# Performance work log

Hardware: AMD Instinct MI355X
Metric: run time of the kernel (lower is better)

The kernel has to match this reference:

```python
import jax, jax.numpy as jnp
import numpy as np

B, M, P = 128, 35, 224  # batch, num Zernike modes, pupil_size
SIGN_PENALTY = 10.0
RECON_WEIGHT = 0.4
DEFOCUS_RAD = 1.0
EPS = 1e-8


def setup_inputs() -> dict:
    key = jax.random.key(0)
    k1, k2, k3, k4 = jax.random.split(key, 4)
    pred = jax.random.normal(k1, (B, M), dtype=jnp.float32)
    target = jax.random.normal(k2, (B, M), dtype=jnp.float32)
    input_psfs = jax.random.uniform(k3, (B, 2, P, P), dtype=jnp.float32)
    zernike_basis = jax.random.normal(k4, (M, P, P), dtype=jnp.float32)
    pupil_mask = jnp.ones((P, P), dtype=jnp.float32)
    return {
        "pred": pred,
        "target": target,
        "input_psfs": input_psfs,
        "zernike_basis": zernike_basis,
        "pupil_mask": pupil_mask,
    }


def _psf_from_phase(phase, pupil_mask):
    # phase: [B,P,P] real; pupil: masked complex field
    pupil = pupil_mask[None, :, :] * jnp.exp(1j * phase)
    field = jnp.fft.fftshift(jnp.fft.fft2(pupil), axes=(-2, -1))
    psf = field.real ** 2 + field.imag ** 2  # |FFT|^2
    psf = psf / (psf.sum(axis=(-2, -1), keepdims=True) + EPS)
    return psf


def reference(pred, target, input_psfs, zernike_basis, pupil_mask):
    # --- sign-weighted MSE on Zernike coefficients ---
    base = (pred - target) ** 2
    sign_match = jnp.sign(pred) * jnp.sign(target)
    weight = jnp.where(sign_match < 0, SIGN_PENALTY, 1.0)
    z_loss = jnp.mean(base * weight)

    # --- batched differentiable PSF reconstruction loss ---
    phase = jnp.einsum('bm,mhw->bhw', pred, zernike_basis)
    phase = phase * pupil_mask[None, :, :]

    sim_if = _psf_from_phase(phase, pupil_mask)  # in-focus

    lin = jnp.linspace(-1.0, 1.0, P, dtype=jnp.float32)
    y, x = jnp.meshgrid(lin, lin, indexing='ij')
    r2 = x ** 2 + y ** 2
    defocus_phase = DEFOCUS_RAD * (2.0 * r2 - 1.0)  # [P,P]
    sim_podf = _psf_from_phase(phase + defocus_phase[None, :, :], pupil_mask)

    # per-sample F.mse_loss then mean over batch == mean over the batched arrays
    recon_loss = (jnp.mean((sim_if - input_psfs[:, 0]) ** 2)
                  + jnp.mean((sim_podf - input_psfs[:, 1]) ** 2))

    return z_loss + RECON_WEIGHT * recon_loss
```

## Files before the change

### kernel.cpp

```cpp
#include <hip/hip_runtime.h>
#include <math.h>

#define BB 128
#define MM 35
#define PSZ 224
#define PP (PSZ*PSZ)
#define SIGN_PENALTY 10.0f
#define RECON_WEIGHT 0.4f
#define DEFOCUS_RAD 1.0f
#define EPS_F 1e-8f
#define INV2PI 0.15915494309189535f


#define WS_PHASE_OFF    2048
#define WS_T_OFF        (WS_PHASE_OFF + BB*PP)
#define N_PARTIALS      (14*BB*2)
#define S1 233
#define S2 20

static constexpr float W16R[16] = {
    1.0f, 0.9238795325f, 0.7071067812f, 0.3826834324f, 0.0f,
    -0.3826834324f, -0.7071067812f, -0.9238795325f, -1.0f,
    -0.9238795325f, -0.7071067812f, -0.3826834324f, 0.0f,
    0.3826834324f, 0.7071067812f, 0.9238795325f};
static constexpr float W16I[16] = {
    0.0f, -0.3826834324f, -0.7071067812f, -0.9238795325f, -1.0f,
    -0.9238795325f, -0.7071067812f, -0.3826834324f, 0.0f,
    0.3826834324f, 0.7071067812f, 0.9238795325f, 1.0f,
    0.9238795325f, 0.7071067812f, 0.3826834324f};
static constexpr float W7R[7] = {
    1.0f, 0.6234898019f, -0.2225209340f, -0.9009688679f,
    -0.9009688679f, -0.2225209340f, 0.6234898019f};
static constexpr float W7I[7] = {
    0.0f, -0.7818314825f, -0.9749279122f, -0.4338837391f,
    0.4338837391f, 0.9749279122f, 0.7818314825f};
static constexpr float W14R[7] = {
    1.0f, 0.9009688679f, 0.6234898019f, 0.2225209340f, -0.2225209340f,
    -0.6234898019f, -0.9009688679f};
static constexpr float W14I[7] = {
    0.0f, -0.4338837391f, -0.7818314825f, -0.9749279122f, -0.9749279122f,
    -0.7818314825f, -0.4338837391f};

__device__ __forceinline__ float lincoord(int i) {
    return -1.0f + 2.0f * (float)i / (float)(PSZ - 1);
}
__device__ __forceinline__ void fast_sincos(float x, float* s, float* c) {
    float rv = x * INV2PI;
    rv -= floorf(rv);
    *s = __builtin_amdgcn_sinf(rv);
    *c = __builtin_amdgcn_cosf(rv);
}
__device__ __forceinline__ float2 wexp_neg(float frac) {
    float rv = -frac;
    rv -= floorf(rv);
    return make_float2(__builtin_amdgcn_cosf(rv), __builtin_amdgcn_sinf(rv));
}
__device__ __forceinline__ unsigned pack_bf2(float a, float b) {
    unsigned r;
    asm("v_cvt_pk_bf16_f32 %0, %1, %2" : "=v"(r) : "v"(a), "v"(b));
    return r;
}
__device__ __forceinline__ float2 unpack_bf2(unsigned v) {
    return make_float2(__uint_as_float(v << 16), __uint_as_float(v & 0xffff0000u));
}
__device__ __forceinline__ float2 cmul(float2 a, float2 b) {
    return make_float2(fmaf(a.x, b.x, -a.y * b.y), fmaf(a.x, b.y, a.y * b.x));
}
__device__ __forceinline__ float2 cmulc(float2 a, float wr, float wi) {
    return make_float2(fmaf(a.x, wr, -a.y * wi), fmaf(a.x, wi, a.y * wr));
}
__device__ __forceinline__ float2 cadd(float2 a, float2 b) {
    return make_float2(a.x + b.x, a.y + b.y);
}
__device__ __forceinline__ float2 csub(float2 a, float2 b) {
    return make_float2(a.x - b.x, a.y - b.y);
}
__device__ __forceinline__ void cfma(float& acc, float c, float v) {
    if (c == 0.f) return;
    if (c == 1.f)  { acc += v; return; }
    if (c == -1.f) { acc -= v; return; }
    acc = fmaf(c, v, acc);
}

__device__ __forceinline__ void dft8_sym(const float2* u, float2* X) {
    float2 a1 = cadd(u[1], u[7]), b1 = csub(u[1], u[7]);
    float2 a2 = cadd(u[2], u[6]), b2 = csub(u[2], u[6]);
    float2 a3 = cadd(u[3], u[5]), b3 = csub(u[3], u[5]);
    float2 s04 = cadd(u[0], u[4]), d04 = csub(u[0], u[4]);
    X[0] = cadd(cadd(s04, a1), cadd(a2, a3));
    X[4] = cadd(csub(s04, a1), csub(a2, a3));
    {
        float2 p = csub(s04, a2);
        float2 q = csub(b1, b3);
        X[2] = make_float2(p.x + q.y, p.y - q.x);
        X[6] = make_float2(p.x - q.y, p.y + q.x);
    }
#pragma unroll
    for (int m = 1; m <= 3; m += 2) {
        float Px = d04.x, Py = d04.y, Qx = 0.f, Qy = 0.f;
#pragma unroll
        for (int n = 1; n <= 3; n++) {
            const float cR = W16R[(2 * n * m) & 15], cI = W16I[(2 * n * m) & 15];
            const float2 a = (n == 1) ? a1 : (n == 2) ? a2 : a3;
            const float2 b = (n == 1) ? b1 : (n == 2) ? b2 : b3;
            cfma(Px, cR, a.x); cfma(Py, cR, a.y);
            cfma(Qx, cI, b.x); cfma(Qy, cI, b.y);
        }
        X[m]     = make_float2(Px - Qy, Py + Qx);
        X[8 - m] = make_float2(Px + Qy, Py - Qx);
    }
}

__device__ __forceinline__ void dft7_sym(const float2* x, float2* X) {
    float2 a1 = cadd(x[1], x[6]), b1 = csub(x[1], x[6]);
    float2 a2 = cadd(x[2], x[5]), b2 = csub(x[2], x[5]);
    float2 a3 = cadd(x[3], x[4]), b3 = csub(x[3], x[4]);
    X[0] = cadd(cadd(x[0], a1), cadd(a2, a3));
#pragma unroll
    for (int k = 1; k <= 3; k++) {
        float Px = x[0].x, Py = x[0].y, Qx = 0.f, Qy = 0.f;
#pragma unroll
        for (int n = 1; n <= 3; n++) {
            const float cR = W7R[(n * k) % 7], cI = W7I[(n * k) % 7];
            const float2 a = (n == 1) ? a1 : (n == 2) ? a2 : a3;
            const float2 b = (n == 1) ? b1 : (n == 2) ? b2 : b3;
            cfma(Px, cR, a.x); cfma(Py, cR, a.y);
            cfma(Qx, cI, b.x); cfma(Qy, cI, b.y);
        }
        X[k]     = make_float2(Px - Qy, Py + Qx);
        X[7 - k] = make_float2(Px + Qy, Py - Qx);
    }
}

__device__ __forceinline__ void inner16_core(const float2* xin,
                                             unsigned* __restrict__ xbuf,
                                             int base, int mul, int n1) {
    float2 u[8], v[8];
#pragma unroll
    for (int n = 0; n < 8; n++) {
        u[n] = cadd(xin[n], xin[n + 8]);
        float2 w = csub(xin[n], xin[n + 8]);
        v[n] = (n == 0) ? w : cmulc(w, W16R[n], W16I[n]);
    }
    float2 u1w = wexp_neg((float)n1 * (1.0f / 224.0f));
    float2 u2w = wexp_neg((float)n1 * (1.0f / 112.0f));
    {
        float2 Xe[8];
        dft8_sym(u, Xe);
        float2 cur = make_float2(1.f, 0.f);
#pragma unroll
        for (int m = 0; m < 8; m++) {
            float2 z = (m == 0) ? Xe[0] : cmul(Xe[m], cur);
            xbuf[base + (14 * (2 * m)) * mul] = pack_bf2(z.x, z.y);
            cur = cmul(cur, u2w);
        }
    }
    {
        float2 Xo[8];
        dft8_sym(v, Xo);
        float2 cur = u1w;
#pragma unroll
        for (int m = 0; m < 8; m++) {
            float2 z = cmul(Xo[m], cur);
            xbuf[base + (14 * (2 * m + 1)) * mul] = pack_bf2(z.x, z.y);
            cur = cmul(cur, u2w);
        }
    }
}

__global__ __launch_bounds__(256) void k_phase(const float* __restrict__ pred,
                                               const float* __restrict__ target,
                                               const float* __restrict__ zern,
                                               const float* __restrict__ mask,
                                               unsigned* __restrict__ field,
                                               float* __restrict__ ws) {
    __shared__ __align__(16) float pl[32 * 36];
    __shared__ float red[256];
    int t = threadIdx.x;
    if (blockIdx.x == 196) {
        int y = blockIdx.y;
        float s = 0.f;
        if (y == 0) {
            if (t < 224) {
                float v = lincoord(t);
                float fc = fmaf(2.f * DEFOCUS_RAD, v * v, -DEFOCUS_RAD);
                float fr = 2.f * DEFOCUS_RAD * v * v;
                float sn, cs;
                fast_sincos(fc, &sn, &cs);
                ((float2*)(ws + 16))[t] = make_float2(cs, sn);
                fast_sincos(fr, &sn, &cs);
                ((float2*)(ws + 512))[t] = make_float2(cs, sn);
            }
            for (int i = t; i < BB * MM; i += 256) {
                float p = pred[i], tg = target[i];
                float dd = p - tg;
                float w = (p * tg < 0.f) ? SIGN_PENALTY : 1.f;
                s = fmaf(dd * dd, w, s);
            }
        } else {
            const int F4 = PP / 4;
            int st = (y - 1) * 4182;
            int en = (y == 3) ? F4 : st + 4182;
            const float4* m4 = (const float4*)mask;
            for (int i = st + t; i < en; i += 256) {
                float4 v = m4[i];
                s = fmaf(v.x, v.x, s); s = fmaf(v.y, v.y, s);
                s = fmaf(v.z, v.z, s); s = fmaf(v.w, v.w, s);
            }
        }
        red[t] = s;
        __syncthreads();
        for (int st = 128; st > 0; st >>= 1) {
            if (t < st) red[t] += red[t + st];
            __syncthreads();
        }
        if (t == 0) {
            if (y == 0) ws[1] = red[0] / (float)(BB * MM);
            else        ws[1 + y] = red[0];
        }
        return;
    }
    int bg = blockIdx.y;
    for (int i = t; i < 32 * MM; i += 256) {
        int j = i / MM, m = i - (i / MM) * MM;
        pl[j * 36 + m] = pred[(bg * 32 + j) * MM + m];
    }
    if (t < 32) pl[t * 36 + 35] = 0.f;
    __syncthreads();
    int pix = blockIdx.x * 256 + t;
    float acc[32];
#pragma unroll
    for (int j = 0; j < 32; j++) acc[j] = 0.f;
    const float4* pl4 = (const float4*)pl;
    for (int mb = 0; mb < 32; mb += 4) {
        float z0 = zern[(size_t)(mb + 0) * PP + pix];
        float z1 = zern[(size_t)(mb + 1) * PP + pix];
        float z2 = zern[(size_t)(mb + 2) * PP + pix];
        float z3 = zern[(size_t)(mb + 3) * PP + pix];
#pragma unroll
        for (int j = 0; j < 32; j++) {
            float4 p4 = pl4[j * 9 + (mb >> 2)];
            acc[j] = fmaf(p4.x, z0, acc[j]);
            acc[j] = fmaf(p4.y, z1, acc[j]);
            acc[j] = fmaf(p4.z, z2, acc[j]);
            acc[j] = fmaf(p4.w, z3, acc[j]);
        }
    }
    {
        float z0 = zern[(size_t)32 * PP + pix];
        float z1 = zern[(size_t)33 * PP + pix];
        float z2 = zern[(size_t)34 * PP + pix];
#pragma unroll
        for (int j = 0; j < 32; j++) {
            float4 p4 = pl4[j * 9 + 8];
            acc[j] = fmaf(p4.x, z0, acc[j]);
            acc[j] = fmaf(p4.y, z1, acc[j]);
            acc[j] = fmaf(p4.z, z2, acc[j]);
        }
    }
    float mk = mask[pix];
#pragma unroll
    for (int j = 0; j < 32; j++) {
        float ph = acc[j] * mk;
        float sn, cs;
        fast_sincos(ph, &sn, &cs);
        field[(size_t)(bg * 32 + j) * PP + pix] = pack_bf2(mk * cs, mk * sn);
    }
}

__global__ __launch_bounds__(256, 5) void k_stage1(const unsigned* __restrict__ field,
                                                   const float* __restrict__ ws,
                                                   unsigned* __restrict__ T) {
    __shared__ unsigned xs[16 * S1];
    int h0 = blockIdx.x * 16;
    int d = blockIdx.y, b = blockIdx.z;
    int t = threadIdx.x;

    if (t < 224) {
        int r = t / 14, n1 = t - (t / 14) * 14;
        const unsigned* frow = field + (size_t)b * PP + (size_t)(h0 + r) * PSZ;
        float2 x0[16];
        if (d) {
            const float2* ctab = (const float2*)(ws + 16);
            const float2* rtab = (const float2*)(ws + 512);
            float2 crow = rtab[h0 + r];
#pragma unroll
            for (int n = 0; n < 16; n++) {
                int col = n1 + 14 * n;
                float2 f = unpack_bf2(frow[col]);
                float2 rot = cmul(crow, ctab[col]);
                x0[n] = cmul(rot, f);
            }
        } else {
#pragma unroll
            for (int n = 0; n < 16; n++) x0[n] = unpack_bf2(frow[n1 + 14 * n]);
        }
        inner16_core(x0, xs, r * S1 + n1, 1, n1);
    }
    __syncthreads();

    {
        int r = t >> 4, k2 = t & 15;
        const unsigned* xr = xs + r * S1 + k2 * 14;
        int img = d * BB + b;
        unsigned* Tt = T + (((size_t)img * 14) * PSZ + (h0 + r)) * 16 + k2;
        float2 e[7], E[7], O[7];
#pragma unroll
        for (int n = 0; n < 7; n++) e[n] = unpack_bf2(xr[2 * n]);
        dft7_sym(e, E);
#pragma unroll
        for (int n = 0; n < 7; n++) e[n] = unpack_bf2(xr[2 * n + 1]);
        dft7_sym(e, O);
#pragma unroll
        for (int k1 = 0; k1 < 7; k1++) {
            float2 op = (k1 == 0) ? O[0] : cmulc(O[k1], W14R[k1], W14I[k1]);
            float2 s = cadd(E[k1], op), q = csub(E[k1], op);
            Tt[(size_t)k1 * (PSZ * 16)]       = pack_bf2(s.x, s.y);
            Tt[(size_t)(k1 + 7) * (PSZ * 16)] = pack_bf2(q.x, q.y);
        }
    }
}

__global__ __launch_bounds__(256, 5) void k_stage2(const unsigned* __restrict__ T,
                                                   const float* __restrict__ psfs,
                                                   const float* __restrict__ ws,
                                                   float* __restrict__ partials) {
    __shared__ unsigned xs[224 * S2];
    __shared__ float red[4];
    int tile = blockIdx.x, b = blockIdx.y, d = blockIdx.z;
    int img = d * BB + b;
    int t = threadIdx.x;
    int k2o = t >> 4, c = t & 15;
    bool act = t < 224;

    const unsigned* Tb = T + ((size_t)img * 14 + tile) * (PSZ * 16);
    const float* inp = psfs + ((size_t)b * 2 + d) * PP;
    int scol = 16 * ((tile + 7) % 14) + c;

    unsigned xr[16];
    if (act) {
#pragma unroll
        for (int n = 0; n < 16; n++) xr[n] = Tb[224 * n + t];
    }
    float pf[14];
#pragma unroll
    for (int j = 0; j < 7; j++) {
        pf[j]     = inp[(size_t)(112 + 16 * j + k2o) * PSZ + scol];
        pf[j + 7] = inp[(size_t)(16 * j + k2o) * PSZ + scol];
    }

    if (act) {
        float2 x[16];
#pragma unroll
        for (int n = 0; n < 16; n++) x[n] = unpack_bf2(xr[n]);
        inner16_core(x, xs, (t >> 4) * S2 + (t & 15), S2, t >> 4);
    }
    __syncthreads();

    float m2 = ws[2] + ws[3] + ws[4];
    float inv_denom = 1.f / (m2 * (float)PP + EPS_F);

    float lsum = 0.f;
    {
        float2 e[7], E[7], O[7];
#pragma unroll
        for (int n = 0; n < 7; n++) e[n] = unpack_bf2(xs[(k2o * 14 + 2 * n) * S2 + c]);
        dft7_sym(e, E);
#pragma unroll
        for (int n = 0; n < 7; n++) e[n] = unpack_bf2(xs[(k2o * 14 + 2 * n + 1) * S2 + c]);
        dft7_sym(e, O);
#pragma unroll
        for (int k1 = 0; k1 < 7; k1++) {
            float2 op = (k1 == 0) ? O[0] : cmulc(O[k1], W14R[k1], W14I[k1]);
            float2 s = cadd(E[k1], op), q = csub(E[k1], op);
            float ds = fmaf(s.x, s.x, s.y * s.y) * inv_denom - pf[k1];
            float dq = fmaf(q.x, q.x, q.y * q.y) * inv_denom - pf[k1 + 7];
            lsum = fmaf(ds, ds, lsum);
            lsum = fmaf(dq, dq, lsum);
        }
    }
#pragma unroll
    for (int off = 32; off > 0; off >>= 1)
        lsum += __shfl_down(lsum, off, 64);
    if ((t & 63) == 0) red[t >> 6] = lsum;
    __syncthreads();
    if (t == 0)
        partials[(blockIdx.z * BB + blockIdx.y) * 14 + blockIdx.x] =
            red[0] + red[1] + red[2] + red[3];
}

__global__ void k_final(const float* __restrict__ ws,
                        const float* __restrict__ partials,
                        float* __restrict__ out) {
    __shared__ float red[256];
    float s = 0.f;
    for (int i = threadIdx.x; i < N_PARTIALS; i += 256) s += partials[i];
    red[threadIdx.x] = s;
    __syncthreads();
    for (int st = 128; st > 0; st >>= 1) {
        if (threadIdx.x < st) red[threadIdx.x] += red[threadIdx.x + st];
        __syncthreads();
    }
    if (threadIdx.x == 0) {
        float recon = red[0] / (float)((size_t)BB * PP);
        out[0] = ws[1] + RECON_WEIGHT * recon;
    }
}

extern "C" void kernel_launch(void* const* d_in, const int* in_sizes, int n_in,
                              void* d_out, int out_size, void* d_ws, size_t ws_size,
                              hipStream_t stream) {
    const float* pred   = (const float*)d_in[0];
    const float* target = (const float*)d_in[1];
    const float* psfs   = (const float*)d_in[2];
    const float* zern   = (const float*)d_in[3];
    const float* mask   = (const float*)d_in[4];

    float*    ws       = (float*)d_ws;
    unsigned* field    = (unsigned*)(ws + WS_PHASE_OFF);
    float*    partials = ws + WS_PHASE_OFF;
    unsigned* T        = (unsigned*)(ws + WS_T_OFF);
    float*    out      = (float*)d_out;

    k_phase<<<dim3(197, 4), 256, 0, stream>>>(pred, target, zern, mask, field, ws);
    k_stage1<<<dim3(14, 2, BB), 256, 0, stream>>>(field, ws, T);
    k_stage2<<<dim3(14, BB, 2), 256, 0, stream>>>(T, psfs, ws, partials);
    k_final<<<1, 256, 0, stream>>>(ws, partials, out);
}
```

Baseline: 153.0 us.

## Fold final reduction into stage2 and register-block two pixels per thread in k_phase

The separate k_final launch is removed. Each k_stage2 block now bumps a global atomic counter after writing its partial sum, and the last block to finish reduces all partials and writes the output. The counter is reset each call by k_phase. k_phase now computes two pixels per thread with software-prefetched Zernike loads, halving its grid; this increases register pressure and reduces the number of blocks in flight.

```diff
diff --git a/kernel.cpp b/kernel.cpp
--- a/kernel.cpp
+++ b/kernel.cpp
@@ -168,19 +168,20 @@
     }
 }
 
-__global__ __launch_bounds__(256) void k_phase(const float* __restrict__ pred,
-                                               const float* __restrict__ target,
-                                               const float* __restrict__ zern,
-                                               const float* __restrict__ mask,
-                                               unsigned* __restrict__ field,
-                                               float* __restrict__ ws) {
+__global__ __launch_bounds__(256, 4) void k_phase(const float* __restrict__ pred,
+                                                  const float* __restrict__ target,
+                                                  const float* __restrict__ zern,
+                                                  const float* __restrict__ mask,
+                                                  unsigned* __restrict__ field,
+                                                  float* __restrict__ ws) {
     __shared__ __align__(16) float pl[32 * 36];
     __shared__ float red[256];
     int t = threadIdx.x;
-    if (blockIdx.x == 196) {
+    if (blockIdx.x == 98) {
         int y = blockIdx.y;
         float s = 0.f;
         if (y == 0) {
+            if (t == 0) ((int*)ws)[8] = 0;
             if (t < 224) {
                 float v = lincoord(t);
                 float fc = fmaf(2.f * DEFOCUS_RAD, v * v, -DEFOCUS_RAD);
@@ -227,44 +228,56 @@
     }
     if (t < 32) pl[t * 36 + 35] = 0.f;
     __syncthreads();
-    int pix = blockIdx.x * 256 + t;
-    float acc[32];
-#pragma unroll
-    for (int j = 0; j < 32; j++) acc[j] = 0.f;
+    int pix0 = blockIdx.x * 512 + t;
+    int pix1 = pix0 + 256;
+    float acc0[32], acc1[32];
+#pragma unroll
+    for (int j = 0; j < 32; j++) { acc0[j] = 0.f; acc1[j] = 0.f; }
     const float4* pl4 = (const float4*)pl;
-    for (int mb = 0; mb < 32; mb += 4) {
-        float z0 = zern[(size_t)(mb + 0) * PP + pix];
-        float z1 = zern[(size_t)(mb + 1) * PP + pix];
-        float z2 = zern[(size_t)(mb + 2) * PP + pix];
-        float z3 = zern[(size_t)(mb + 3) * PP + pix];
+    float cz[4], cw[4];
+#pragma unroll
+    for (int q = 0; q < 4; q++) {
+        cz[q] = zern[(size_t)q * PP + pix0];
+        cw[q] = zern[(size_t)q * PP + pix1];
+    }
+    for (int ch = 0; ch < 9; ch++) {
+        float nz[4], nw[4];
+        if (ch < 8) {
+            int nb = (ch + 1) * 4;
+#pragma unroll
+            for (int q = 0; q < 4; q++) {
+                if (nb + q < MM) {
+                    nz[q] = zern[(size_t)(nb + q) * PP + pix0];
+                    nw[q] = zern[(size_t)(nb + q) * PP + pix1];
+                } else { nz[q] = 0.f; nw[q] = 0.f; }
+            }
+        }
 #pragma unroll
         for (int j = 0; j < 32; j++) {
-            float4 p4 = pl4[j * 9 + (mb >> 2)];
-            acc[j] = fmaf(p4.x, z0, acc[j]);
-            acc[j] = fmaf(p4.y, z1, acc[j]);
-            acc[j] = fmaf(p4.z, z2, acc[j]);
-            acc[j] = fmaf(p4.w, z3, acc[j]);
-        }
-    }
-    {
-        float z0 = zern[(size_t)32 * PP + pix];
-        float z1 = zern[(size_t)33 * PP + pix];
-        float z2 = zern[(size_t)34 * PP + pix];
-#pragma unroll
-        for (int j = 0; j < 32; j++) {
-            float4 p4 = pl4[j * 9 + 8];
-            acc[j] = fmaf(p4.x, z0, acc[j]);
-            acc[j] = fmaf(p4.y, z1, acc[j]);
-            acc[j] = fmaf(p4.z, z2, acc[j]);
-        }
-    }
-    float mk = mask[pix];
+            float4 p4 = pl4[j * 9 + ch];
+            acc0[j] = fmaf(p4.x, cz[0], acc0[j]);
+            acc0[j] = fmaf(p4.y, cz[1], acc0[j]);
+            acc0[j] = fmaf(p4.z, cz[2], acc0[j]);
+            acc0[j] = fmaf(p4.w, cz[3], acc0[j]);
+            acc1[j] = fmaf(p4.x, cw[0], acc1[j]);
+            acc1[j] = fmaf(p4.y, cw[1], acc1[j]);
+            acc1[j] = fmaf(p4.z, cw[2], acc1[j]);
+            acc1[j] = fmaf(p4.w, cw[3], acc1[j]);
+        }
+        if (ch < 8) {
+#pragma unroll
+            for (int q = 0; q < 4; q++) { cz[q] = nz[q]; cw[q] = nw[q]; }
+        }
+    }
+    float mk0 = mask[pix0], mk1 = mask[pix1];
 #pragma unroll
     for (int j = 0; j < 32; j++) {
-        float ph = acc[j] * mk;
+        size_t row = (size_t)(bg * 32 + j) * PP;
         float sn, cs;
-        fast_sincos(ph, &sn, &cs);
-        field[(size_t)(bg * 32 + j) * PP + pix] = pack_bf2(mk * cs, mk * sn);
+        fast_sincos(acc0[j] * mk0, &sn, &cs);
+        field[row + pix0] = pack_bf2(mk0 * cs, mk0 * sn);
+        fast_sincos(acc1[j] * mk1, &sn, &cs);
+        field[row + pix1] = pack_bf2(mk1 * cs, mk1 * sn);
     }
 }
 
@@ -323,10 +336,12 @@
 
 __global__ __launch_bounds__(256, 5) void k_stage2(const unsigned* __restrict__ T,
                                                    const float* __restrict__ psfs,
-                                                   const float* __restrict__ ws,
-                                                   float* __restrict__ partials) {
+                                                   float* __restrict__ ws,
+                                                   float* __restrict__ partials,
+                                                   float* __restrict__ out) {
     __shared__ unsigned xs[224 * S2];
     __shared__ float red[4];
+    __shared__ int lastflag;
     int tile = blockIdx.x, b = blockIdx.y, d = blockIdx.z;
     int img = d * BB + b;
     int t = threadIdx.x;
@@ -384,26 +399,28 @@
         lsum += __shfl_down(lsum, off, 64);
     if ((t & 63) == 0) red[t >> 6] = lsum;
     __syncthreads();
-    if (t == 0)
+    if (t == 0) {
         partials[(blockIdx.z * BB + blockIdx.y) * 14 + blockIdx.x] =
             red[0] + red[1] + red[2] + red[3];
-}
-
-__global__ void k_final(const float* __restrict__ ws,
-                        const float* __restrict__ partials,
-                        float* __restrict__ out) {
-    __shared__ float red[256];
-    float s = 0.f;
-    for (int i = threadIdx.x; i < N_PARTIALS; i += 256) s += partials[i];
-    red[threadIdx.x] = s;
+        __threadfence();
+        int old = atomicAdd((int*)ws + 8, 1);
+        lastflag = (old == N_PARTIALS - 1);
+    }
     __syncthreads();
-    for (int st = 128; st > 0; st >>= 1) {
-        if (threadIdx.x < st) red[threadIdx.x] += red[threadIdx.x + st];
+    if (lastflag) {
+        __threadfence();
+        float s = 0.f;
+        for (int i = t; i < N_PARTIALS; i += 256) s += partials[i];
+#pragma unroll
+        for (int off = 32; off > 0; off >>= 1)
+            s += __shfl_down(s, off, 64);
+        if ((t & 63) == 0) red[t >> 6] = s;
         __syncthreads();
-    }
-    if (threadIdx.x == 0) {
-        float recon = red[0] / (float)((size_t)BB * PP);
-        out[0] = ws[1] + RECON_WEIGHT * recon;
+        if (t == 0) {
+            float recon = (red[0] + red[1] + red[2] + red[3]) /
+                          (float)((size_t)BB * PP);
+            out[0] = ws[1] + RECON_WEIGHT * recon;
+        }
     }
 }
 
@@ -422,8 +439,7 @@
     unsigned* T        = (unsigned*)(ws + WS_T_OFF);
     float*    out      = (float*)d_out;
 
-    k_phase<<<dim3(197, 4), 256, 0, stream>>>(pred, target, zern, mask, field, ws);
+    k_phase<<<dim3(99, 4), 256, 0, stream>>>(pred, target, zern, mask, field, ws);
     k_stage1<<<dim3(14, 2, BB), 256, 0, stream>>>(field, ws, T);
-    k_stage2<<<dim3(14, BB, 2), 256, 0, stream>>>(T, psfs, ws, partials);
-    k_final<<<1, 256, 0, stream>>>(ws, partials, out);
-}
+    k_stage2<<<dim3(14, BB, 2), 256, 0, stream>>>(T, psfs, ws, partials, out);
+}
```

New measurement: 288.2 us. 88.3% more time.
